# Kernel tuning notes

Hardware: AMD Instinct MI355X
Metric: run time of the kernel (lower is better)

Reference implementation:

```python
import jax, jax.numpy as jnp
import numpy as np

N, E, NFEAT, H = 100000, 1600000, 128, 128
NLAYER = 3


def setup_inputs() -> dict:
    key = jax.random.key(0)
    ks = jax.random.split(key, 20)
    s = 0.05
    return {
        "features": jax.random.normal(ks[0], (N, NFEAT), jnp.float32),
        "edge_index": jax.random.randint(ks[1], (2, E), 0, N, jnp.int32),
        "edge_weight": jax.random.uniform(ks[2], (E,), jnp.float32),
        "w1": jax.random.normal(ks[3], (H, NFEAT), jnp.float32) * s,
        "b1": jnp.zeros((H,), jnp.float32),
        "gin_w1": jax.random.normal(ks[4], (NLAYER, H, H), jnp.float32) * s,
        "gin_b1": jnp.zeros((NLAYER, H), jnp.float32),
        "gin_w2": jax.random.normal(ks[5], (NLAYER, H, H), jnp.float32) * s,
        "gin_b2": jnp.zeros((NLAYER, H), jnp.float32),
        "gru_wih": jax.random.normal(ks[6], (NLAYER, 3 * H, H), jnp.float32) * s,
        "gru_whh": jax.random.normal(ks[7], (NLAYER, 3 * H, H), jnp.float32) * s,
        "gru_bih": jnp.zeros((NLAYER, 3 * H), jnp.float32),
        "gru_bhh": jnp.zeros((NLAYER, 3 * H), jnp.float32),
        "head_w1": jax.random.normal(ks[8], (NLAYER, H, H), jnp.float32) * s,
        "head_b1": jnp.zeros((NLAYER, H), jnp.float32),
        "head_w2_0": jax.random.normal(ks[9], (2, H), jnp.float32) * s,
        "head_b2_0": jnp.zeros((2,), jnp.float32),
        "head_w2_1": jax.random.normal(ks[10], (6, H), jnp.float32) * s,
        "head_b2_1": jnp.zeros((6,), jnp.float32),
        "head_w2_2": jax.random.normal(ks[11], (21, H), jnp.float32) * s,
        "head_b2_2": jnp.zeros((21,), jnp.float32),
    }


def _gru_cell(x, h, wih, whh, bih, bhh):
    # torch.nn.GRUCell semantics
    gi = x @ wih.T + bih           # [N, 3H]
    gh = h @ whh.T + bhh           # [N, 3H]
    ir, iz, inn = jnp.split(gi, 3, axis=1)
    hr, hz, hn = jnp.split(gh, 3, axis=1)
    r = jax.nn.sigmoid(ir + hr)
    z = jax.nn.sigmoid(iz + hz)
    n = jnp.tanh(inn + r * hn)
    return (1.0 - z) * n + z * h


def reference(features, edge_index, edge_weight, w1, b1,
              gin_w1, gin_b1, gin_w2, gin_b2,
              gru_wih, gru_whh, gru_bih, gru_bhh,
              head_w1, head_b1,
              head_w2_0, head_b2_0, head_w2_1, head_b2_1, head_w2_2, head_b2_2):
    n_nodes = features.shape[0]
    dst, src = edge_index[0], edge_index[1]  # spmm: out[dst] += w * x[src]
    head_w2 = [head_w2_0, head_w2_1, head_w2_2]
    head_b2 = [head_b2_0, head_b2_1, head_b2_2]

    x = jax.nn.relu(features @ w1.T + b1)  # mlp1 + ReLU
    layer_info = x
    outputs, _outputs = [], []
    for i in range(NLAYER):
        agg = jax.ops.segment_sum(edge_weight[:, None] * x[src], dst,
                                  num_segments=n_nodes)
        h = _gru_cell(agg, layer_info, gru_wih[i], gru_whh[i],
                      gru_bih[i], gru_bhh[i])
        # GinMlp: Linear -> ReLU -> Linear, then outer ReLU
        x = jax.nn.relu(h @ gin_w1[i].T + gin_b1[i]) @ gin_w2[i].T + gin_b2[i]
        x = jax.nn.relu(x)
        # custom layer-norm variant
        x = x / jnp.sqrt(1.0 + jnp.sum(x * x, axis=1, keepdims=True))
        # prediction head for this layer (mlpPos = [0,1,2])
        tmp = jax.nn.relu(x @ head_w1[i].T + head_b1[i]) @ head_w2[i].T + head_b2[i]
        outputs.append(jax.nn.log_softmax(tmp, axis=1))
        _outputs.append(jax.nn.softmax(tmp, axis=1))
        layer_info = x
    return tuple(outputs) + tuple(_outputs)
```

## Files before the change

kernel.cpp:

```cpp
#include <hip/hip_runtime.h>
#include <cstdint>
#include <cstddef>


typedef short  v8s __attribute__((ext_vector_type(8)));
typedef float  v4f __attribute__((ext_vector_type(4)));

#define STREAM_CAP 512

static __device__ __forceinline__ float bf2f(uint16_t u) {
  return __uint_as_float(((uint32_t)u) << 16);
}
static __device__ __forceinline__ uint16_t f2b(float f) {
  uint32_t x = __float_as_uint(f);
  return (uint16_t)((x + 0x7FFFu + ((x >> 16) & 1u)) >> 16);
}
static __device__ __forceinline__ float sigmoidf_(float v) {
  return 1.f / (1.f + __expf(-v));
}
static __device__ __forceinline__ float tanhf_(float v) {
  return 1.f - 2.f / (__expf(2.f * v) + 1.f);
}

__global__ void k_detect(const uint32_t* __restrict__ u, int* __restrict__ flag) {
  int lane = threadIdx.x;
  uint32_t low = u[lane] & 0xFFFFu;
  uint32_t e = (low >> 7) & 0xFFu;
  bool pass = (e == 0) || (e >= 110 && e <= 141);
  unsigned long long b = __ballot(pass);
  if (lane == 0) *flag = (__popcll(b) >= 32) ? 1 : 0;
}

struct CvtDesc {
  const void* src[18];
  int off[19];
};

__global__ void k_cvtw(CvtDesc c, float* __restrict__ wbase,
                       uint16_t* __restrict__ wb16,
                       const int* __restrict__ flag, int total) {
  int gid = blockIdx.x * 256 + threadIdx.x;
  if (gid >= total) return;
  int t = 0;
#pragma unroll
  for (int i = 1; i < 18; i++)
    if (gid >= c.off[i]) t = i;
  int local = gid - c.off[t];
  float v;
  if (*flag) v = bf2f(((const uint16_t*)c.src[t])[local]);
  else       v = ((const float*)c.src[t])[local];
  wbase[gid] = v;
  wb16[gid] = f2b(v);
}

__global__ void k_cvt_feat(const void* __restrict__ src, uint16_t* __restrict__ dst,
                           int n, const int* __restrict__ flag) {
  int i = blockIdx.x * 256 + threadIdx.x;
  if (i >= n) return;
  if (*flag) dst[i] = ((const uint16_t*)src)[i];
  else       dst[i] = f2b(((const float*)src)[i]);
}

__global__ void k_zero_i(int* __restrict__ p, int n) {
  int i = blockIdx.x * 256 + threadIdx.x;
  if (i < n) p[i] = 0;
}

__global__ void k_zero_f(float* __restrict__ p, int n) {
  int i = blockIdx.x * 256 + threadIdx.x;
  if (i < n) p[i] = 0.f;
}

__global__ void k_pack_mm(const uint16_t* __restrict__ src, uint16_t* __restrict__ dst,
                          int nmat) {
  int id = blockIdx.x * 256 + threadIdx.x;
  if (id >= nmat * 2048) return;
  int mat = id >> 11;
  int rem = id & 2047;
  int blk = rem >> 6, lane = rem & 63;
  int kc = blk >> 3, t = blk & 7;
  int n0 = lane & 15, quad = lane >> 4;
  const uint16_t* s = src + (size_t)mat * 16384 + (size_t)(t * 16 + n0) * 128 + kc * 32 + quad * 8;
  uint16_t* d = dst + (size_t)id * 8;
  *reinterpret_cast<v8s*>(d) = *reinterpret_cast<const v8s*>(s);
}

__global__ void k_pack_gru(const uint16_t* __restrict__ wih, const uint16_t* __restrict__ whh,
                           uint16_t* __restrict__ dst, int nlayer) {
  int id = blockIdx.x * 256 + threadIdx.x;
  if (id >= nlayer * 192 * 64) return;
  int lane = id & 63;
  int blk = (id >> 6) % 192;
  int layer = (id >> 6) / 192;
  int g = blk % 3;
  int mat = (blk / 3) % 2;
  int u = (blk / 6) % 2;
  int w = (blk / 12) % 4;
  int kc = blk / 48;
  int n0 = lane & 15, quad = lane >> 4;
  const uint16_t* base = (mat == 0 ? wih : whh) + (size_t)layer * 384 * 128;
  const uint16_t* s = base + (size_t)(g * 128 + w * 32 + u * 16 + n0) * 128 + kc * 32 + quad * 8;
  uint16_t* d = dst + ((size_t)layer * 192 + blk) * 512 + (size_t)lane * 8;
  *reinterpret_cast<v8s*>(d) = *reinterpret_cast<const v8s*>(s);
}

__global__ void k_scatter1(const int* __restrict__ dst, const int* __restrict__ src,
                           const void* __restrict__ w, int* __restrict__ bcnt,
                           uint2* __restrict__ ep0, const int* __restrict__ flag, int E) {
  int e = blockIdx.x * 256 + threadIdx.x;
  if (e < E) {
    int d = dst[e];
    int sid = (d >> 7) * 8 + (blockIdx.x & 7);
    int pos = atomicAdd(&bcnt[sid], 1);
    if (pos >= STREAM_CAP) pos = STREAM_CAP - 1;
    float wv;
    if (*flag) wv = bf2f(((const uint16_t*)w)[e]);
    else       wv = ((const float*)w)[e];
    ep0[(size_t)sid * STREAM_CAP + pos] =
        make_uint2((uint32_t)src[e] | (((uint32_t)d & 127u) << 25),
                   __float_as_uint(wv));
  }
}

__global__ void k_bprefix(const int* __restrict__ bcnt, int* __restrict__ bbase,
                          int nbuckets) {
  __shared__ int red[256];
  int t = threadIdx.x;
  int chunk = (nbuckets + 255) >> 8;
  int beg = t * chunk;
  int end = beg + chunk;
  if (end > nbuckets) end = nbuckets;
  int s = 0;
  for (int b = beg; b < end; b++) {
    int tot = 0;
#pragma unroll
    for (int j = 0; j < 8; j++) {
      int c = bcnt[b * 8 + j];
      if (c > STREAM_CAP) c = STREAM_CAP;
      tot += c;
    }
    bbase[b] = tot;
    s += tot;
  }
  red[t] = s;
  __syncthreads();
  for (int off = 1; off < 256; off <<= 1) {
    int u = (t >= off) ? red[t - off] : 0;
    __syncthreads();
    red[t] += u;
    __syncthreads();
  }
  int run = red[t] - s;
  for (int b = beg; b < end; b++) {
    int tot = bbase[b];
    bbase[b] = run;
    run += tot;
  }
}

__global__ void k_build(const uint2* __restrict__ ep0, const int* __restrict__ bcnt,
                        const int* __restrict__ bbase, int* __restrict__ rowptr,
                        uint2* __restrict__ ep, int n, int nbuckets) {
  __shared__ int lcnt[128];
  __shared__ int lbase[128];
  __shared__ int cnts[8];
  int b = blockIdx.x, t = threadIdx.x;
  if (t < 128) lcnt[t] = 0;
  if (t < 8) {
    int c = bcnt[b * 8 + t];
    cnts[t] = (c > STREAM_CAP) ? STREAM_CAP : c;
  }
  __syncthreads();

  for (int j = 0; j < 8; j++) {
    int c = cnts[j];
    const uint2* sp = ep0 + (size_t)(b * 8 + j) * STREAM_CAP;
    for (int p = t; p < c; p += 256) {
      uint2 v = sp[p];
      atomicAdd(&lcnt[v.x >> 25], 1);
    }
  }
  __syncthreads();

  if (t < 128) lbase[t] = lcnt[t];
  __syncthreads();
  for (int off = 1; off < 128; off <<= 1) {
    int v = 0;
    if (t < 128 && t >= off) v = lbase[t - off];
    __syncthreads();
    if (t < 128) lbase[t] += v;
    __syncthreads();
  }

  int base = bbase[b];
  if (t < 128) {
    int excl = lbase[t] - lcnt[t];
    int node = b * 128 + t;
    if (node < n) rowptr[node] = base + excl;
    lcnt[t] = base + excl;
  }
  if (b == nbuckets - 1 && t == 0) rowptr[n] = base + lbase[127];
  __syncthreads();

  for (int j = 0; j < 8; j++) {
    int c = cnts[j];
    const uint2* sp = ep0 + (size_t)(b * 8 + j) * STREAM_CAP;
    for (int p = t; p < c; p += 256) {
      uint2 v = sp[p];
      int pos = atomicAdd(&lcnt[v.x >> 25], 1);
      ep[pos] = make_uint2(v.x & 0x01FFFFFFu, v.y);
    }
  }
}

__global__ void k_spmm(const uint16_t* __restrict__ x, const int* __restrict__ rowptr,
                       const uint2* __restrict__ ep, uint16_t* __restrict__ agg, int n) {
  int node = blockIdx.x * 4 + (threadIdx.x >> 6);
  int lane = threadIdx.x & 63;
  if (node >= n) return;
  int p0 = rowptr[node], p1 = rowptr[node + 1];
  float a0 = 0.f, a1 = 0.f;
  int p = p0;
  for (; p + 3 < p1; p += 4) {
    uint2 e0 = ep[p], e1 = ep[p + 1], e2 = ep[p + 2], e3 = ep[p + 3];
    uint32_t u0 = *reinterpret_cast<const uint32_t*>(x + (size_t)e0.x * 128 + lane * 2);
    uint32_t u1 = *reinterpret_cast<const uint32_t*>(x + (size_t)e1.x * 128 + lane * 2);
    uint32_t u2 = *reinterpret_cast<const uint32_t*>(x + (size_t)e2.x * 128 + lane * 2);
    uint32_t u3 = *reinterpret_cast<const uint32_t*>(x + (size_t)e3.x * 128 + lane * 2);
    float w0 = __uint_as_float(e0.y), w1 = __uint_as_float(e1.y);
    float w2 = __uint_as_float(e2.y), w3 = __uint_as_float(e3.y);
    a0 = fmaf(w0, bf2f((uint16_t)u0), a0);
    a1 = fmaf(w0, bf2f((uint16_t)(u0 >> 16)), a1);
    a0 = fmaf(w1, bf2f((uint16_t)u1), a0);
    a1 = fmaf(w1, bf2f((uint16_t)(u1 >> 16)), a1);
    a0 = fmaf(w2, bf2f((uint16_t)u2), a0);
    a1 = fmaf(w2, bf2f((uint16_t)(u2 >> 16)), a1);
    a0 = fmaf(w3, bf2f((uint16_t)u3), a0);
    a1 = fmaf(w3, bf2f((uint16_t)(u3 >> 16)), a1);
  }
  for (; p < p1; p++) {
    uint2 e0 = ep[p];
    float w0 = __uint_as_float(e0.y);
    uint32_t u0 = *reinterpret_cast<const uint32_t*>(x + (size_t)e0.x * 128 + lane * 2);
    a0 = fmaf(w0, bf2f((uint16_t)u0), a0);
    a1 = fmaf(w0, bf2f((uint16_t)(u0 >> 16)), a1);
  }
  uint32_t packed = (uint32_t)f2b(a0) | ((uint32_t)f2b(a1) << 16);
  *reinterpret_cast<uint32_t*>(agg + (size_t)node * 128 + lane * 2) = packed;
}

template <int EPI>
__launch_bounds__(256)
__global__ void k_mm(const uint16_t* __restrict__ A, const uint16_t* __restrict__ Wrp,
                     const float* __restrict__ bias, uint16_t* __restrict__ C,
                     int nrows) {
  int wave = threadIdx.x >> 6, lane = threadIdx.x & 63;
  int n0 = lane & 15, quad = lane >> 4;
  int m0 = (blockIdx.x * 4 + wave) * 32;
  int r0 = m0 + n0, r1 = m0 + 16 + n0;
  bool ok0 = r0 < nrows, ok1 = r1 < nrows;
  const v8s z8 = {0, 0, 0, 0, 0, 0, 0, 0};

  v4f acc[2][8];
#pragma unroll
  for (int rt = 0; rt < 2; rt++)
#pragma unroll
    for (int t = 0; t < 8; t++) acc[rt][t] = {0.f, 0.f, 0.f, 0.f};

  const uint16_t* ap0 = A + (size_t)r0 * 128 + quad * 8;
  const uint16_t* ap1 = A + (size_t)r1 * 128 + quad * 8;
#pragma unroll
  for (int kc = 0; kc < 4; kc++) {
    v8s a0 = ok0 ? *reinterpret_cast<const v8s*>(ap0 + kc * 32) : z8;
    v8s a1 = ok1 ? *reinterpret_cast<const v8s*>(ap1 + kc * 32) : z8;
    const uint16_t* wp = Wrp + (size_t)kc * 4096 + (size_t)lane * 8;
#pragma unroll
    for (int t = 0; t < 8; t++) {
      v8s bf = *reinterpret_cast<const v8s*>(wp + t * 512);
      acc[0][t] = __builtin_amdgcn_mfma_f32_16x16x32_bf16(a0, bf, acc[0][t], 0, 0, 0);
      acc[1][t] = __builtin_amdgcn_mfma_f32_16x16x32_bf16(a1, bf, acc[1][t], 0, 0, 0);
    }
  }

#pragma unroll
  for (int rt = 0; rt < 2; rt++) {
    int mb = m0 + rt * 16;
    float vv[8][4];
#pragma unroll
    for (int t = 0; t < 8; t++) {
      float b = bias[t * 16 + n0];
#pragma unroll
      for (int r = 0; r < 4; r++) vv[t][r] = fmaxf(acc[rt][t][r] + b, 0.f);
    }
    if (EPI == 2) {
#pragma unroll
      for (int r = 0; r < 4; r++) {
        float ss = 0.f;
#pragma unroll
        for (int t = 0; t < 8; t++) ss = fmaf(vv[t][r], vv[t][r], ss);
        ss += __shfl_xor(ss, 1);
        ss += __shfl_xor(ss, 2);
        ss += __shfl_xor(ss, 4);
        ss += __shfl_xor(ss, 8);
        float sc = rsqrtf(1.f + ss);
#pragma unroll
        for (int t = 0; t < 8; t++) vv[t][r] *= sc;
      }
    }
#pragma unroll
    for (int r = 0; r < 4; r++) {
      int row = mb + quad * 4 + r;
      if (row >= nrows) continue;
#pragma unroll
      for (int t = 0; t < 8; t++)
        C[(size_t)row * 128 + t * 16 + n0] = f2b(vv[t][r]);
    }
  }
}

__launch_bounds__(256)
__global__ void k_mm12(const uint16_t* __restrict__ A, const uint16_t* __restrict__ W1rp,
                       const float* __restrict__ b1, const uint16_t* __restrict__ W2rp,
                       const float* __restrict__ b2, uint16_t* __restrict__ C,
                       int nrows) {
  __shared__ uint16_t hl[128][136];
  int wave = threadIdx.x >> 6, lane = threadIdx.x & 63;
  int n0 = lane & 15, quad = lane >> 4;
  int m0 = (blockIdx.x * 4 + wave) * 32;
  int r0 = m0 + n0, r1 = m0 + 16 + n0;
  bool ok0 = r0 < nrows, ok1 = r1 < nrows;
  const v8s z8 = {0, 0, 0, 0, 0, 0, 0, 0};

  v4f acc[2][8];
#pragma unroll
  for (int rt = 0; rt < 2; rt++)
#pragma unroll
    for (int t = 0; t < 8; t++) acc[rt][t] = {0.f, 0.f, 0.f, 0.f};

  const uint16_t* ap0 = A + (size_t)r0 * 128 + quad * 8;
  const uint16_t* ap1 = A + (size_t)r1 * 128 + quad * 8;
#pragma unroll
  for (int kc = 0; kc < 4; kc++) {
    v8s a0 = ok0 ? *reinterpret_cast<const v8s*>(ap0 + kc * 32) : z8;
    v8s a1 = ok1 ? *reinterpret_cast<const v8s*>(ap1 + kc * 32) : z8;
    const uint16_t* wp = W1rp + (size_t)kc * 4096 + (size_t)lane * 8;
#pragma unroll
    for (int t = 0; t < 8; t++) {
      v8s bf = *reinterpret_cast<const v8s*>(wp + t * 512);
      acc[0][t] = __builtin_amdgcn_mfma_f32_16x16x32_bf16(a0, bf, acc[0][t], 0, 0, 0);
      acc[1][t] = __builtin_amdgcn_mfma_f32_16x16x32_bf16(a1, bf, acc[1][t], 0, 0, 0);
    }
  }

#pragma unroll
  for (int rt = 0; rt < 2; rt++) {
#pragma unroll
    for (int t = 0; t < 8; t++) {
      float b = b1[t * 16 + n0];
#pragma unroll
      for (int r = 0; r < 4; r++) {
        int rl = wave * 32 + rt * 16 + quad * 4 + r;
        hl[rl][t * 16 + n0] = f2b(fmaxf(acc[rt][t][r] + b, 0.f));
      }
    }
  }
  __syncthreads();

  v4f acc2[2][8];
#pragma unroll
  for (int rt = 0; rt < 2; rt++)
#pragma unroll
    for (int t = 0; t < 8; t++) acc2[rt][t] = {0.f, 0.f, 0.f, 0.f};

#pragma unroll
  for (int kc = 0; kc < 4; kc++) {
    v8s a0 = *reinterpret_cast<const v8s*>(&hl[wave * 32 + n0][kc * 32 + quad * 8]);
    v8s a1 = *reinterpret_cast<const v8s*>(&hl[wave * 32 + 16 + n0][kc * 32 + quad * 8]);
    const uint16_t* wp = W2rp + (size_t)kc * 4096 + (size_t)lane * 8;
#pragma unroll
    for (int t = 0; t < 8; t++) {
      v8s bf = *reinterpret_cast<const v8s*>(wp + t * 512);
      acc2[0][t] = __builtin_amdgcn_mfma_f32_16x16x32_bf16(a0, bf, acc2[0][t], 0, 0, 0);
      acc2[1][t] = __builtin_amdgcn_mfma_f32_16x16x32_bf16(a1, bf, acc2[1][t], 0, 0, 0);
    }
  }

#pragma unroll
  for (int rt = 0; rt < 2; rt++) {
    int mb = m0 + rt * 16;
    float vv[8][4];
#pragma unroll
    for (int t = 0; t < 8; t++) {
      float b = b2[t * 16 + n0];
#pragma unroll
      for (int r = 0; r < 4; r++) vv[t][r] = fmaxf(acc2[rt][t][r] + b, 0.f);
    }
#pragma unroll
    for (int r = 0; r < 4; r++) {
      float ss = 0.f;
#pragma unroll
      for (int t = 0; t < 8; t++) ss = fmaf(vv[t][r], vv[t][r], ss);
      ss += __shfl_xor(ss, 1);
      ss += __shfl_xor(ss, 2);
      ss += __shfl_xor(ss, 4);
      ss += __shfl_xor(ss, 8);
      float sc = rsqrtf(1.f + ss);
#pragma unroll
      for (int t = 0; t < 8; t++) vv[t][r] *= sc;
    }
#pragma unroll
    for (int r = 0; r < 4; r++) {
      int row = mb + quad * 4 + r;
      if (row >= nrows) continue;
#pragma unroll
      for (int t = 0; t < 8; t++)
        C[(size_t)row * 128 + t * 16 + n0] = f2b(vv[t][r]);
    }
  }
}

__launch_bounds__(256)
__global__ void k_gru(const uint16_t* __restrict__ agg, const uint16_t* __restrict__ xb,
                      const uint16_t* __restrict__ Wrp,
                      const float* __restrict__ bih, const float* __restrict__ bhh,
                      uint16_t* __restrict__ hb, int n, int ntiles, int nrb) {
  __shared__ uint16_t wl[48][512];
  int i = blockIdx.x;
  int s = (i >> 3) & 3;
  int rb = (i >> 5) * 8 + (i & 7);
  int wave = threadIdx.x >> 6, lane = threadIdx.x & 63;
  int n0 = lane & 15, quad = lane >> 4;
  const v8s z8 = {0, 0, 0, 0, 0, 0, 0, 0};

  for (int c = threadIdx.x; c < 3072; c += 256) {
    int f = c >> 6;
    int w8 = (c & 63) << 3;
    int kc = f / 12, j = f % 12;
    const uint16_t* g = Wrp + (size_t)((kc * 4 + s) * 12 + j) * 512 + w8;
    *reinterpret_cast<v8s*>(&wl[f][w8]) = *reinterpret_cast<const v8s*>(g);
  }
  __syncthreads();

  float bi_r[2], bi_z[2], bi_n[2], bh_r[2], bh_z[2], bh_n[2];
#pragma unroll
  for (int u = 0; u < 2; u++) {
    int col = s * 32 + u * 16 + n0;
    bi_r[u] = bih[col]; bi_z[u] = bih[128 + col]; bi_n[u] = bih[256 + col];
    bh_r[u] = bhh[col]; bh_z[u] = bhh[128 + col]; bh_n[u] = bhh[256 + col];
  }

  for (int t = rb; t < ntiles; t += nrb) {
    int m0 = t * 128 + wave * 32;
    int r0 = m0 + n0, r1 = m0 + 16 + n0;
    bool ok0 = r0 < n, ok1 = r1 < n;

    v4f accI[2][2][3], accH[2][2][3];
#pragma unroll
    for (int rt = 0; rt < 2; rt++)
#pragma unroll
      for (int u = 0; u < 2; u++)
#pragma unroll
        for (int g = 0; g < 3; g++) {
          accI[rt][u][g] = {0.f, 0.f, 0.f, 0.f};
          accH[rt][u][g] = {0.f, 0.f, 0.f, 0.f};
        }

    const uint16_t* ap0 = agg + (size_t)r0 * 128 + quad * 8;
    const uint16_t* ap1 = agg + (size_t)r1 * 128 + quad * 8;
    const uint16_t* xp0 = xb + (size_t)r0 * 128 + quad * 8;
    const uint16_t* xp1 = xb + (size_t)r1 * 128 + quad * 8;
#pragma unroll
    for (int kc = 0; kc < 4; kc++) {
      v8s a0 = ok0 ? *reinterpret_cast<const v8s*>(ap0 + kc * 32) : z8;
      v8s a1 = ok1 ? *reinterpret_cast<const v8s*>(ap1 + kc * 32) : z8;
      v8s x0 = ok0 ? *reinterpret_cast<const v8s*>(xp0 + kc * 32) : z8;
      v8s x1 = ok1 ? *reinterpret_cast<const v8s*>(xp1 + kc * 32) : z8;
#pragma unroll
      for (int u = 0; u < 2; u++) {
#pragma unroll
        for (int g = 0; g < 3; g++) {
          v8s bi = *reinterpret_cast<const v8s*>(&wl[kc * 12 + u * 6 + g][(size_t)lane * 8]);
          v8s bh = *reinterpret_cast<const v8s*>(&wl[kc * 12 + u * 6 + 3 + g][(size_t)lane * 8]);
          accI[0][u][g] = __builtin_amdgcn_mfma_f32_16x16x32_bf16(a0, bi, accI[0][u][g], 0, 0, 0);
          accI[1][u][g] = __builtin_amdgcn_mfma_f32_16x16x32_bf16(a1, bi, accI[1][u][g], 0, 0, 0);
          accH[0][u][g] = __builtin_amdgcn_mfma_f32_16x16x32_bf16(x0, bh, accH[0][u][g], 0, 0, 0);
          accH[1][u][g] = __builtin_amdgcn_mfma_f32_16x16x32_bf16(x1, bh, accH[1][u][g], 0, 0, 0);
        }
      }
    }

#pragma unroll
    for (int rt = 0; rt < 2; rt++) {
#pragma unroll
      for (int u = 0; u < 2; u++) {
        int col = s * 32 + u * 16 + n0;
#pragma unroll
        for (int r = 0; r < 4; r++) {
          int row = m0 + rt * 16 + quad * 4 + r;
          if (row < n) {
            float ir = accI[rt][u][0][r] + bi_r[u];
            float iz = accI[rt][u][1][r] + bi_z[u];
            float in_ = accI[rt][u][2][r] + bi_n[u];
            float hr = accH[rt][u][0][r] + bh_r[u];
            float hz = accH[rt][u][1][r] + bh_z[u];
            float hn = accH[rt][u][2][r] + bh_n[u];
            float rr = sigmoidf_(ir + hr);
            float zz = sigmoidf_(iz + hz);
            float nn = tanhf_(fmaf(rr, hn, in_));
            float xv = bf2f(xb[(size_t)row * 128 + col]);
            hb[(size_t)row * 128 + col] = f2b(fmaf(zz, xv - nn, nn));
          }
        }
      }
    }
  }
}

template <int C>
__launch_bounds__(256)
__global__ void k_mmh(const uint16_t* __restrict__ A, const uint16_t* __restrict__ Wrp,
                      const float* __restrict__ bias,
                      const float* __restrict__ w2, const float* __restrict__ b2,
                      float* __restrict__ out_log, float* __restrict__ out_soft,
                      int nrows) {
  __shared__ uint16_t hl[128][130];
  int wave = threadIdx.x >> 6, lane = threadIdx.x & 63;
  int n0 = lane & 15, quad = lane >> 4;
  int m0 = (blockIdx.x * 4 + wave) * 32;
  int r0 = m0 + n0, r1 = m0 + 16 + n0;
  bool ok0 = r0 < nrows, ok1 = r1 < nrows;
  const v8s z8 = {0, 0, 0, 0, 0, 0, 0, 0};

  v4f acc[2][8];
#pragma unroll
  for (int rt = 0; rt < 2; rt++)
#pragma unroll
    for (int t = 0; t < 8; t++) acc[rt][t] = {0.f, 0.f, 0.f, 0.f};

  const uint16_t* ap0 = A + (size_t)r0 * 128 + quad * 8;
  const uint16_t* ap1 = A + (size_t)r1 * 128 + quad * 8;
#pragma unroll
  for (int kc = 0; kc < 4; kc++) {
    v8s a0 = ok0 ? *reinterpret_cast<const v8s*>(ap0 + kc * 32) : z8;
    v8s a1 = ok1 ? *reinterpret_cast<const v8s*>(ap1 + kc * 32) : z8;
    const uint16_t* wp = Wrp + (size_t)kc * 4096 + (size_t)lane * 8;
#pragma unroll
    for (int t = 0; t < 8; t++) {
      v8s bf = *reinterpret_cast<const v8s*>(wp + t * 512);
      acc[0][t] = __builtin_amdgcn_mfma_f32_16x16x32_bf16(a0, bf, acc[0][t], 0, 0, 0);
      acc[1][t] = __builtin_amdgcn_mfma_f32_16x16x32_bf16(a1, bf, acc[1][t], 0, 0, 0);
    }
  }

#pragma unroll
  for (int rt = 0; rt < 2; rt++) {
#pragma unroll
    for (int t = 0; t < 8; t++) {
      float b = bias[t * 16 + n0];
#pragma unroll
      for (int r = 0; r < 4; r++) {
        int rl = wave * 32 + rt * 16 + quad * 4 + r;
        hl[rl][t * 16 + n0] = f2b(fmaxf(acc[rt][t][r] + b, 0.f));
      }
    }
  }
  __syncthreads();

  int tid = threadIdx.x;
  if (tid < 128) {
    int node = blockIdx.x * 128 + tid;
    if (node < nrows) {
      float lg[C];
#pragma unroll
      for (int c = 0; c < C; c++) lg[c] = b2[c];
      for (int k = 0; k < 64; k++) {
        uint32_t u = *reinterpret_cast<const uint32_t*>(&hl[tid][2 * k]);
        float x0 = bf2f((uint16_t)u);
        float x1 = bf2f((uint16_t)(u >> 16));
#pragma unroll
        for (int c = 0; c < C; c++) lg[c] = fmaf(x0, w2[c * 128 + 2 * k], lg[c]);
#pragma unroll
        for (int c = 0; c < C; c++) lg[c] = fmaf(x1, w2[c * 128 + 2 * k + 1], lg[c]);
      }
      float m = lg[0];
#pragma unroll
      for (int c = 1; c < C; c++) m = fmaxf(m, lg[c]);
      float sum = 0.f;
      float e[C];
#pragma unroll
      for (int c = 0; c < C; c++) { e[c] = __expf(lg[c] - m); sum += e[c]; }
      float ls = __logf(sum);
      float inv = 1.f / sum;
#pragma unroll
      for (int c = 0; c < C; c++) {
        out_log[(size_t)node * C + c] = lg[c] - m - ls;
        out_soft[(size_t)node * C + c] = e[c] * inv;
      }
    }
  }
}

extern "C" void kernel_launch(void* const* d_in, const int* in_sizes, int n_in,
                              void* d_out, int out_size, void* d_ws, size_t ws_size,
                              hipStream_t stream) {
  const int N = in_sizes[0] / 128;
  const int E = in_sizes[2];
  const int NB = (N + 127) >> 7;
  const int NS = NB * 8;

  static const int wn[18] = {16384, 128, 49152, 384, 49152, 384,
                             147456, 147456, 1152, 1152, 49152, 384,
                             256, 2, 768, 6, 2688, 21};
  CvtDesc cd;
  int off = 0;
  for (int i = 0; i < 18; i++) {
    cd.src[i] = d_in[3 + i];
    cd.off[i] = off;
    off += wn[i];
  }
  cd.off[18] = off;
  const int wtotal = off;

  char* p = (char*)d_ws;
  size_t used = 0;
  auto alloc = [&](size_t bytes) -> char* {
    char* r = p;
    size_t b = (bytes + 255) & ~(size_t)255;
    p += b;
    used += b;
    return r;
  };
  int*      flag    = (int*)alloc(256);
  float*    wbase   = (float*)alloc((size_t)wtotal * 4);
  uint16_t* wb16    = (uint16_t*)alloc((size_t)wtotal * 2);
  uint16_t* mmrp    = (uint16_t*)alloc((size_t)10 * 16384 * 2);
  uint16_t* grurp   = (uint16_t*)alloc((size_t)3 * 192 * 512 * 2);
  uint16_t* xb      = (uint16_t*)alloc((size_t)N * 128 * 2);
  uint16_t* aggb    = (uint16_t*)alloc((size_t)N * 128 * 2);
  uint16_t* hb      = (uint16_t*)alloc((size_t)N * 128 * 2);
  int*      rowptr  = (int*)alloc((size_t)(N + 1) * 4);
  int*      bcnt    = (int*)alloc((size_t)NS * 4);
  int*      bbase   = (int*)alloc((size_t)(NB + 1) * 4);
  uint2*    ep0     = (uint2*)alloc((size_t)NS * STREAM_CAP * 8);
  uint2*    epack   = (uint2*)alloc((size_t)E * 8);

  float* out = (float*)d_out;
  float* outlog[3]  = {out, out + 2 * (size_t)N, out + 8 * (size_t)N};
  float* outsoft[3] = {out + 29 * (size_t)N, out + 31 * (size_t)N, out + 37 * (size_t)N};

  if (used > ws_size) {
    k_zero_f<<<(out_size + 255) / 256, 256, 0, stream>>>(out, out_size);
    return;
  }

  float* b1f   = wbase + cd.off[1];
  float* ginb1 = wbase + cd.off[3];
  float* ginb2 = wbase + cd.off[5];
  float* bih   = wbase + cd.off[8];
  float* bhh   = wbase + cd.off[9];
  float* hb1   = wbase + cd.off[11];
  float* hw2_0 = wbase + cd.off[12];
  float* hb2_0 = wbase + cd.off[13];
  float* hw2_1 = wbase + cd.off[14];
  float* hb2_1 = wbase + cd.off[15];
  float* hw2_2 = wbase + cd.off[16];
  float* hb2_2 = wbase + cd.off[17];

  uint16_t* w1b   = wb16 + cd.off[0];
  uint16_t* ginw1b= wb16 + cd.off[2];
  uint16_t* ginw2b= wb16 + cd.off[4];
  uint16_t* wihb  = wb16 + cd.off[6];
  uint16_t* whhb  = wb16 + cd.off[7];
  uint16_t* hw1b  = wb16 + cd.off[10];

  uint16_t* w1rp    = mmrp;
  uint16_t* ginw1rp = mmrp + (size_t)1 * 16384;
  uint16_t* ginw2rp = mmrp + (size_t)4 * 16384;
  uint16_t* hw1rp   = mmrp + (size_t)7 * 16384;

  const int* dst = (const int*)d_in[1];
  const int* src = (const int*)d_in[1] + E;

  k_detect<<<1, 64, 0, stream>>>((const uint32_t*)d_in[0], flag);
  k_cvtw<<<(wtotal + 255) / 256, 256, 0, stream>>>(cd, wbase, wb16, flag, wtotal);
  k_cvt_feat<<<((size_t)N * 128 + 255) / 256, 256, 0, stream>>>(d_in[0], aggb,
                                                                N * 128, flag);
  k_pack_mm<<<(1 * 2048 + 255) / 256, 256, 0, stream>>>(w1b, w1rp, 1);
  k_pack_mm<<<(3 * 2048 + 255) / 256, 256, 0, stream>>>(ginw1b, ginw1rp, 3);
  k_pack_mm<<<(3 * 2048 + 255) / 256, 256, 0, stream>>>(ginw2b, ginw2rp, 3);
  k_pack_mm<<<(3 * 2048 + 255) / 256, 256, 0, stream>>>(hw1b, hw1rp, 3);
  k_pack_gru<<<(3 * 192 * 64 + 255) / 256, 256, 0, stream>>>(wihb, whhb, grurp, 3);

  k_zero_i<<<(NS + 255) / 256, 256, 0, stream>>>(bcnt, NS);
  k_scatter1<<<(E + 255) / 256, 256, 0, stream>>>(dst, src, d_in[2], bcnt,
                                                  ep0, flag, E);
  k_bprefix<<<1, 256, 0, stream>>>(bcnt, bbase, NB);
  k_build<<<NB, 256, 0, stream>>>(ep0, bcnt, bbase, rowptr, epack, N, NB);

  int mmrb = (N + 127) / 128;
  int spb  = (N + 3) / 4;
  int ntiles = (N + 127) / 128;
  const int NRB = 192;

  k_mm<1><<<mmrb, 256, 0, stream>>>(aggb, w1rp, b1f, xb, N);

  for (int i = 0; i < 3; i++) {
    k_spmm<<<spb, 256, 0, stream>>>(xb, rowptr, epack, aggb, N);
    k_gru<<<4 * NRB, 256, 0, stream>>>(aggb, xb, grurp + (size_t)i * 192 * 512,
                                       bih + i * 384, bhh + i * 384, hb, N,
                                       ntiles, NRB);
    k_mm12<<<mmrb, 256, 0, stream>>>(hb, ginw1rp + (size_t)i * 16384,
                                     ginb1 + i * 128,
                                     ginw2rp + (size_t)i * 16384,
                                     ginb2 + i * 128, xb, N);
    if (i == 0)
      k_mmh<2><<<mmrb, 256, 0, stream>>>(xb, hw1rp, hb1, hw2_0, hb2_0,
                                         outlog[0], outsoft[0], N);
    else if (i == 1)
      k_mmh<6><<<mmrb, 256, 0, stream>>>(xb, hw1rp + (size_t)16384, hb1 + 128,
                                         hw2_1, hb2_1, outlog[1], outsoft[1], N);
    else
      k_mmh<21><<<mmrb, 256, 0, stream>>>(xb, hw1rp + (size_t)2 * 16384, hb1 + 256,
                                          hw2_2, hb2_2, outlog[2], outsoft[2], N);
  }
}
```

Measured before the change: 886.5 us.

## Rewrite edge bucketing with block-local histograms and register-resident GRU weights

The edge partition now builds a per-block shared-memory histogram and reserves contiguous space per bucket with one global atomic per bucket, replacing per-edge global atomics over eight streams. The CSR build then reads one contiguous region per bucket. The GRU kernel is restructured so each of 8 waves holds its slice of W_ih/W_hh in registers (24 fragments) instead of staging it in LDS, and processes 32-row tiles over a persistent 256-block grid. The aim is to cut atomic contention and LDS traffic. In exchange, register pressure rises, and a bucket that overflows its cap of 4096 edges would be silently clamped.

```diff
diff --git a/kernel.cpp b/kernel.cpp
--- a/kernel.cpp
+++ b/kernel.cpp
@@ -6,7 +6,7 @@
 typedef short  v8s __attribute__((ext_vector_type(8)));
 typedef float  v4f __attribute__((ext_vector_type(4)));
 
-#define STREAM_CAP 512
+#define BUCKET_CAP 4096
 
 static __device__ __forceinline__ float bf2f(uint16_t u) {
   return __uint_as_float(((uint32_t)u) << 16);
@@ -104,25 +104,42 @@
   *reinterpret_cast<v8s*>(d) = *reinterpret_cast<const v8s*>(s);
 }
 
-__global__ void k_scatter1(const int* __restrict__ dst, const int* __restrict__ src,
-                           const void* __restrict__ w, int* __restrict__ bcnt,
-                           uint2* __restrict__ ep0, const int* __restrict__ flag, int E) {
-  int e = blockIdx.x * 256 + threadIdx.x;
-  if (e < E) {
+__global__ void k_part(const int* __restrict__ dst, const int* __restrict__ src,
+                       const void* __restrict__ w, int* __restrict__ gcur,
+                       uint2* __restrict__ ep0, const int* __restrict__ flag,
+                       int E, int NB) {
+  __shared__ int hist[1024];
+  __shared__ int lbase[1024];
+  int t = threadIdx.x;
+  int CH = (E + gridDim.x - 1) / gridDim.x;
+  int e0 = blockIdx.x * CH;
+  int e1 = e0 + CH;
+  if (e1 > E) e1 = E;
+  for (int b = t; b < NB; b += 256) hist[b] = 0;
+  __syncthreads();
+  for (int e = e0 + t; e < e1; e += 256)
+    atomicAdd(&hist[dst[e] >> 7], 1);
+  __syncthreads();
+  for (int b = t; b < NB; b += 256) {
+    int c = hist[b];
+    lbase[b] = c ? atomicAdd(&gcur[b], c) : 0;
+    hist[b] = 0;
+  }
+  __syncthreads();
+  bool bf = (*flag) != 0;
+  for (int e = e0 + t; e < e1; e += 256) {
     int d = dst[e];
-    int sid = (d >> 7) * 8 + (blockIdx.x & 7);
-    int pos = atomicAdd(&bcnt[sid], 1);
-    if (pos >= STREAM_CAP) pos = STREAM_CAP - 1;
-    float wv;
-    if (*flag) wv = bf2f(((const uint16_t*)w)[e]);
-    else       wv = ((const float*)w)[e];
-    ep0[(size_t)sid * STREAM_CAP + pos] =
+    int b = d >> 7;
+    int pos = lbase[b] + atomicAdd(&hist[b], 1);
+    if (pos >= BUCKET_CAP) pos = BUCKET_CAP - 1;
+    float wv = bf ? bf2f(((const uint16_t*)w)[e]) : ((const float*)w)[e];
+    ep0[(size_t)b * BUCKET_CAP + pos] =
         make_uint2((uint32_t)src[e] | (((uint32_t)d & 127u) << 25),
                    __float_as_uint(wv));
   }
 }
 
-__global__ void k_bprefix(const int* __restrict__ bcnt, int* __restrict__ bbase,
+__global__ void k_bprefix(const int* __restrict__ gcur, int* __restrict__ bbase,
                           int nbuckets) {
   __shared__ int red[256];
   int t = threadIdx.x;
@@ -132,15 +149,10 @@
   if (end > nbuckets) end = nbuckets;
   int s = 0;
   for (int b = beg; b < end; b++) {
-    int tot = 0;
-#pragma unroll
-    for (int j = 0; j < 8; j++) {
-      int c = bcnt[b * 8 + j];
-      if (c > STREAM_CAP) c = STREAM_CAP;
-      tot += c;
-    }
-    bbase[b] = tot;
-    s += tot;
+    int c = gcur[b];
+    if (c > BUCKET_CAP) c = BUCKET_CAP;
+    bbase[b] = c;
+    s += c;
   }
   red[t] = s;
   __syncthreads();
@@ -158,58 +170,46 @@
   }
 }
 
-__global__ void k_build(const uint2* __restrict__ ep0, const int* __restrict__ bcnt,
+__global__ void k_build(const uint2* __restrict__ ep0, const int* __restrict__ gcur,
                         const int* __restrict__ bbase, int* __restrict__ rowptr,
                         uint2* __restrict__ ep, int n, int nbuckets) {
   __shared__ int lcnt[128];
-  __shared__ int lbase[128];
-  __shared__ int cnts[8];
+  __shared__ int lsc[128];
   int b = blockIdx.x, t = threadIdx.x;
+  int cnt = gcur[b];
+  if (cnt > BUCKET_CAP) cnt = BUCKET_CAP;
   if (t < 128) lcnt[t] = 0;
-  if (t < 8) {
-    int c = bcnt[b * 8 + t];
-    cnts[t] = (c > STREAM_CAP) ? STREAM_CAP : c;
-  }
-  __syncthreads();
-
-  for (int j = 0; j < 8; j++) {
-    int c = cnts[j];
-    const uint2* sp = ep0 + (size_t)(b * 8 + j) * STREAM_CAP;
-    for (int p = t; p < c; p += 256) {
-      uint2 v = sp[p];
-      atomicAdd(&lcnt[v.x >> 25], 1);
-    }
-  }
-  __syncthreads();
-
-  if (t < 128) lbase[t] = lcnt[t];
+  __syncthreads();
+
+  const uint2* sp = ep0 + (size_t)b * BUCKET_CAP;
+  for (int p = t; p < cnt; p += 256)
+    atomicAdd(&lcnt[sp[p].x >> 25], 1);
+  __syncthreads();
+
+  if (t < 128) lsc[t] = lcnt[t];
   __syncthreads();
   for (int off = 1; off < 128; off <<= 1) {
     int v = 0;
-    if (t < 128 && t >= off) v = lbase[t - off];
+    if (t < 128 && t >= off) v = lsc[t - off];
     __syncthreads();
-    if (t < 128) lbase[t] += v;
+    if (t < 128) lsc[t] += v;
     __syncthreads();
   }
 
   int base = bbase[b];
   if (t < 128) {
-    int excl = lbase[t] - lcnt[t];
+    int excl = lsc[t] - lcnt[t];
     int node = b * 128 + t;
     if (node < n) rowptr[node] = base + excl;
     lcnt[t] = base + excl;
   }
-  if (b == nbuckets - 1 && t == 0) rowptr[n] = base + lbase[127];
-  __syncthreads();
-
-  for (int j = 0; j < 8; j++) {
-    int c = cnts[j];
-    const uint2* sp = ep0 + (size_t)(b * 8 + j) * STREAM_CAP;
-    for (int p = t; p < c; p += 256) {
-      uint2 v = sp[p];
-      int pos = atomicAdd(&lcnt[v.x >> 25], 1);
-      ep[pos] = make_uint2(v.x & 0x01FFFFFFu, v.y);
-    }
+  if (b == nbuckets - 1 && t == 0) rowptr[n] = base + lsc[127];
+  __syncthreads();
+
+  for (int p = t; p < cnt; p += 256) {
+    uint2 v = sp[p];
+    int pos = atomicAdd(&lcnt[v.x >> 25], 1);
+    ep[pos] = make_uint2(v.x & 0x01FFFFFFu, v.y);
   }
 }
 
@@ -419,51 +419,44 @@
   }
 }
 
-__launch_bounds__(256)
-__global__ void k_gru(const uint16_t* __restrict__ agg, const uint16_t* __restrict__ xb,
-                      const uint16_t* __restrict__ Wrp,
-                      const float* __restrict__ bih, const float* __restrict__ bhh,
-                      uint16_t* __restrict__ hb, int n, int ntiles, int nrb) {
-  __shared__ uint16_t wl[48][512];
-  int i = blockIdx.x;
-  int s = (i >> 3) & 3;
-  int rb = (i >> 5) * 8 + (i & 7);
+__launch_bounds__(512, 2)
+__global__ void k_gru8(const uint16_t* __restrict__ agg, const uint16_t* __restrict__ xb,
+                       const uint16_t* __restrict__ Wrp,
+                       const float* __restrict__ bih, const float* __restrict__ bhh,
+                       uint16_t* __restrict__ hb, int n, int ntiles) {
   int wave = threadIdx.x >> 6, lane = threadIdx.x & 63;
   int n0 = lane & 15, quad = lane >> 4;
+  int s = wave >> 1, u = wave & 1;
   const v8s z8 = {0, 0, 0, 0, 0, 0, 0, 0};
 
-  for (int c = threadIdx.x; c < 3072; c += 256) {
-    int f = c >> 6;
-    int w8 = (c & 63) << 3;
-    int kc = f / 12, j = f % 12;
-    const uint16_t* g = Wrp + (size_t)((kc * 4 + s) * 12 + j) * 512 + w8;
-    *reinterpret_cast<v8s*>(&wl[f][w8]) = *reinterpret_cast<const v8s*>(g);
-  }
-  __syncthreads();
-
-  float bi_r[2], bi_z[2], bi_n[2], bh_r[2], bh_z[2], bh_n[2];
-#pragma unroll
-  for (int u = 0; u < 2; u++) {
-    int col = s * 32 + u * 16 + n0;
-    bi_r[u] = bih[col]; bi_z[u] = bih[128 + col]; bi_n[u] = bih[256 + col];
-    bh_r[u] = bhh[col]; bh_z[u] = bhh[128 + col]; bh_n[u] = bhh[256 + col];
-  }
-
-  for (int t = rb; t < ntiles; t += nrb) {
-    int m0 = t * 128 + wave * 32;
+  v8s wf[24];
+#pragma unroll
+  for (int kc = 0; kc < 4; kc++)
+#pragma unroll
+    for (int mat = 0; mat < 2; mat++)
+#pragma unroll
+      for (int g = 0; g < 3; g++)
+        wf[kc * 6 + mat * 3 + g] = *reinterpret_cast<const v8s*>(
+            Wrp + (size_t)((kc * 4 + s) * 12 + (u * 2 + mat) * 3 + g) * 512 +
+            (size_t)lane * 8);
+
+  int col = wave * 16 + n0;
+  float bir = bih[col], biz = bih[128 + col], bin = bih[256 + col];
+  float bhr = bhh[col], bhz = bhh[128 + col], bhn = bhh[256 + col];
+
+  for (int tt = blockIdx.x; tt < ntiles; tt += gridDim.x) {
+    int m0 = tt * 32;
     int r0 = m0 + n0, r1 = m0 + 16 + n0;
     bool ok0 = r0 < n, ok1 = r1 < n;
 
-    v4f accI[2][2][3], accH[2][2][3];
+    v4f accI[2][3], accH[2][3];
 #pragma unroll
     for (int rt = 0; rt < 2; rt++)
 #pragma unroll
-      for (int u = 0; u < 2; u++)
-#pragma unroll
-        for (int g = 0; g < 3; g++) {
-          accI[rt][u][g] = {0.f, 0.f, 0.f, 0.f};
-          accH[rt][u][g] = {0.f, 0.f, 0.f, 0.f};
-        }
+      for (int g = 0; g < 3; g++) {
+        accI[rt][g] = {0.f, 0.f, 0.f, 0.f};
+        accH[rt][g] = {0.f, 0.f, 0.f, 0.f};
+      }
 
     const uint16_t* ap0 = agg + (size_t)r0 * 128 + quad * 8;
     const uint16_t* ap1 = agg + (size_t)r1 * 128 + quad * 8;
@@ -476,40 +469,31 @@
       v8s x0 = ok0 ? *reinterpret_cast<const v8s*>(xp0 + kc * 32) : z8;
       v8s x1 = ok1 ? *reinterpret_cast<const v8s*>(xp1 + kc * 32) : z8;
 #pragma unroll
-      for (int u = 0; u < 2; u++) {
-#pragma unroll
-        for (int g = 0; g < 3; g++) {
-          v8s bi = *reinterpret_cast<const v8s*>(&wl[kc * 12 + u * 6 + g][(size_t)lane * 8]);
-          v8s bh = *reinterpret_cast<const v8s*>(&wl[kc * 12 + u * 6 + 3 + g][(size_t)lane * 8]);
-          accI[0][u][g] = __builtin_amdgcn_mfma_f32_16x16x32_bf16(a0, bi, accI[0][u][g], 0, 0, 0);
-          accI[1][u][g] = __builtin_amdgcn_mfma_f32_16x16x32_bf16(a1, bi, accI[1][u][g], 0, 0, 0);
-          accH[0][u][g] = __builtin_amdgcn_mfma_f32_16x16x32_bf16(x0, bh, accH[0][u][g], 0, 0, 0);
-          accH[1][u][g] = __builtin_amdgcn_mfma_f32_16x16x32_bf16(x1, bh, accH[1][u][g], 0, 0, 0);
-        }
+      for (int g = 0; g < 3; g++) {
+        accI[0][g] = __builtin_amdgcn_mfma_f32_16x16x32_bf16(a0, wf[kc * 6 + g], accI[0][g], 0, 0, 0);
+        accI[1][g] = __builtin_amdgcn_mfma_f32_16x16x32_bf16(a1, wf[kc * 6 + g], accI[1][g], 0, 0, 0);
+        accH[0][g] = __builtin_amdgcn_mfma_f32_16x16x32_bf16(x0, wf[kc * 6 + 3 + g], accH[0][g], 0, 0, 0);
+        accH[1][g] = __builtin_amdgcn_mfma_f32_16x16x32_bf16(x1, wf[kc * 6 + 3 + g], accH[1][g], 0, 0, 0);
       }
     }
 
 #pragma unroll
     for (int rt = 0; rt < 2; rt++) {
 #pragma unroll
-      for (int u = 0; u < 2; u++) {
-        int col = s * 32 + u * 16 + n0;
-#pragma unroll
-        for (int r = 0; r < 4; r++) {
-          int row = m0 + rt * 16 + quad * 4 + r;
-          if (row < n) {
-            float ir = accI[rt][u][0][r] + bi_r[u];
-            float iz = accI[rt][u][1][r] + bi_z[u];
-            float in_ = accI[rt][u][2][r] + bi_n[u];
-            float hr = accH[rt][u][0][r] + bh_r[u];
-            float hz = accH[rt][u][1][r] + bh_z[u];
-            float hn = accH[rt][u][2][r] + bh_n[u];
-            float rr = sigmoidf_(ir + hr);
-            float zz = sigmoidf_(iz + hz);
-            float nn = tanhf_(fmaf(rr, hn, in_));
-            float xv = bf2f(xb[(size_t)row * 128 + col]);
-            hb[(size_t)row * 128 + col] = f2b(fmaf(zz, xv - nn, nn));
-          }
+      for (int r = 0; r < 4; r++) {
+        int row = m0 + rt * 16 + quad * 4 + r;
+        if (row < n) {
+          float ir = accI[rt][0][r] + bir;
+          float iz = accI[rt][1][r] + biz;
+          float in_ = accI[rt][2][r] + bin;
+          float hr = accH[rt][0][r] + bhr;
+          float hz = accH[rt][1][r] + bhz;
+          float hn = accH[rt][2][r] + bhn;
+          float rr = sigmoidf_(ir + hr);
+          float zz = sigmoidf_(iz + hz);
+          float nn = tanhf_(fmaf(rr, hn, in_));
+          float xv = bf2f(xb[(size_t)row * 128 + col]);
+          hb[(size_t)row * 128 + col] = f2b(fmaf(zz, xv - nn, nn));
         }
       }
     }
@@ -606,7 +590,6 @@
   const int N = in_sizes[0] / 128;
   const int E = in_sizes[2];
   const int NB = (N + 127) >> 7;
-  const int NS = NB * 8;
 
   static const int wn[18] = {16384, 128, 49152, 384, 49152, 384,
                              147456, 147456, 1152, 1152, 49152, 384,
@@ -639,9 +622,9 @@
   uint16_t* aggb    = (uint16_t*)alloc((size_t)N * 128 * 2);
   uint16_t* hb      = (uint16_t*)alloc((size_t)N * 128 * 2);
   int*      rowptr  = (int*)alloc((size_t)(N + 1) * 4);
-  int*      bcnt    = (int*)alloc((size_t)NS * 4);
+  int*      gcur    = (int*)alloc((size_t)NB * 4);
   int*      bbase   = (int*)alloc((size_t)(NB + 1) * 4);
-  uint2*    ep0     = (uint2*)alloc((size_t)NS * STREAM_CAP * 8);
+  uint2*    ep0     = (uint2*)alloc((size_t)NB * BUCKET_CAP * 8);
   uint2*    epack   = (uint2*)alloc((size_t)E * 8);
 
   float* out = (float*)d_out;
@@ -691,24 +674,21 @@
   k_pack_mm<<<(3 * 2048 + 255) / 256, 256, 0, stream>>>(hw1b, hw1rp, 3);
   k_pack_gru<<<(3 * 192 * 64 + 255) / 256, 256, 0, stream>>>(wihb, whhb, grurp, 3);
 
-  k_zero_i<<<(NS + 255) / 256, 256, 0, stream>>>(bcnt, NS);
-  k_scatter1<<<(E + 255) / 256, 256, 0, stream>>>(dst, src, d_in[2], bcnt,
-                                                  ep0, flag, E);
-  k_bprefix<<<1, 256, 0, stream>>>(bcnt, bbase, NB);
-  k_build<<<NB, 256, 0, stream>>>(ep0, bcnt, bbase, rowptr, epack, N, NB);
+  k_zero_i<<<(NB + 255) / 256, 256, 0, stream>>>(gcur, NB);
+  k_part<<<256, 256, 0, stream>>>(dst, src, d_in[2], gcur, ep0, flag, E, NB);
+  k_bprefix<<<1, 256, 0, stream>>>(gcur, bbase, NB);
+  k_build<<<NB, 256, 0, stream>>>(ep0, gcur, bbase, rowptr, epack, N, NB);
 
   int mmrb = (N + 127) / 128;
   int spb  = (N + 3) / 4;
-  int ntiles = (N + 127) / 128;
-  const int NRB = 192;
+  int ntiles32 = (N + 31) / 32;
 
   k_mm<1><<<mmrb, 256, 0, stream>>>(aggb, w1rp, b1f, xb, N);
 
   for (int i = 0; i < 3; i++) {
     k_spmm<<<spb, 256, 0, stream>>>(xb, rowptr, epack, aggb, N);
-    k_gru<<<4 * NRB, 256, 0, stream>>>(aggb, xb, grurp + (size_t)i * 192 * 512,
-                                       bih + i * 384, bhh + i * 384, hb, N,
-                                       ntiles, NRB);
+    k_gru8<<<256, 512, 0, stream>>>(aggb, xb, grurp + (size_t)i * 192 * 512,
+                                    bih + i * 384, bhh + i * 384, hb, N, ntiles32);
     k_mm12<<<mmrb, 256, 0, stream>>>(hb, ginw1rp + (size_t)i * 16384,
                                      ginb1 + i * 128,
                                      ginw2rp + (size_t)i * 16384,
```

Measured after the change: 829.7 us. -6.4%, faster.
